# Performance work log

Measured on AMD Instinct MI355X. Metric: run time of the kernel, lower is better.

Reference implementation:

```python
import jax, jax.numpy as jnp
import numpy as np

B, L, D_MODEL, N_HEAD = 8, 1024, 1024, 16
D_K = D_MODEL // N_HEAD  # 64


def setup_inputs() -> dict:
    key = jax.random.key(0)
    ks = jax.random.split(key, 10)
    scale = 1.0 / np.sqrt(D_MODEL)
    inp = {
        "q": jax.random.normal(ks[0], (B, L, D_MODEL), jnp.float32),
        "k": jax.random.normal(ks[1], (B, L, D_MODEL), jnp.float32),
        "v": jax.random.normal(ks[2], (B, L, D_MODEL), jnp.float32),
        "mask": jax.random.randint(ks[3], (B, L, L), 0, 2, jnp.int32),
        # per-head projection weights stacked: [H, d_model, d_k]
        "Wq": jax.random.normal(ks[4], (N_HEAD, D_MODEL, D_K), jnp.float32) * scale,
        "Wk": jax.random.normal(ks[5], (N_HEAD, D_MODEL, D_K), jnp.float32) * scale,
        "Wv": jax.random.normal(ks[6], (N_HEAD, D_MODEL, D_K), jnp.float32) * scale,
        # output projection (Dense with bias): [d_model, d_model], [d_model]
        "Wo": jax.random.normal(ks[7], (D_MODEL, D_MODEL), jnp.float32) * scale,
        "bo": jnp.zeros((D_MODEL,), jnp.float32),
    }
    return inp


def reference(q, k, v, mask, Wq, Wk, Wv, Wo, bo):
    d_k = Wq.shape[-1]
    # per-head projections (mode=1 per-head Dense, no bias), vectorized over heads
    qs = jnp.einsum('bld,hdk->bhlk', q, Wq)  # [B,H,Lq,d_k]
    ks = jnp.einsum('bld,hdk->bhlk', k, Wk)  # [B,H,Lk,d_k]
    vs = jnp.einsum('bld,hdk->bhlk', v, Wv)  # [B,H,Lk,d_v]
    # scaled dot-product attention: batch_dot(q,k,axes=[2,2]) / sqrt(d_k)
    scores = jnp.einsum('bhqd,bhkd->bhqk', qs, ks) / jnp.sqrt(jnp.float32(d_k))
    # additive mask: -1e9 * (1 - mask), broadcast over heads
    scores = scores + (-1e9 * (1.0 - mask.astype(jnp.float32)))[:, None, :, :]
    attn = jax.nn.softmax(scores, axis=-1)           # [B,H,Lq,Lk] (dropout inactive at inference)
    head = jnp.einsum('bhqk,bhkd->bhqd', attn, vs)   # [B,H,Lq,d_v]
    b, h, lq, dv = head.shape
    # Concatenate heads along feature axis (head index major, as in mode=1 Concatenate)
    head_cat = head.transpose(0, 2, 1, 3).reshape(b, lq, h * dv)
    outputs = head_cat @ Wo + bo                     # [B,Lq,d_model] (dropout inactive)
    # attn heads also concatenated along last axis in mode=1
    attn_cat = attn.transpose(0, 2, 1, 3).reshape(b, lq, h * attn.shape[-1])
    return outputs, attn_cat
```

## Files before the change

### kernel.cpp

```cpp
#include <hip/hip_runtime.h>

typedef _Float16 f16;
typedef _Float16 f16x8 __attribute__((ext_vector_type(8)));
typedef _Float16 f16x4 __attribute__((ext_vector_type(4)));
typedef _Float16 f16x2 __attribute__((ext_vector_type(2)));
typedef float f32x4 __attribute__((ext_vector_type(4)));

#define GLOAD_LDS16(g, l) \
    __builtin_amdgcn_global_load_lds((const __attribute__((address_space(1))) void*)(g), \
                                     (__attribute__((address_space(3))) void*)(l), 16, 0, 0)

__device__ __forceinline__ f16x2 cvt_pk_f16(float a, float b) {
    return __builtin_bit_cast(f16x2, __builtin_amdgcn_cvt_pkrtz(a, b));
}

#define SC_LOG2E 0.180336880f

__global__ __launch_bounds__(256) void cvt3_kernel(const float* __restrict__ q,
        const float* __restrict__ k, const float* __restrict__ v, f16* __restrict__ out) {
    const int z = blockIdx.y;
    const float* src = (z == 0) ? q : (z == 1) ? k : v;
    const size_t i = ((size_t)blockIdx.x * 256 + threadIdx.x) * 8;
    float4 a = *(const float4*)&src[i], b2 = *(const float4*)&src[i + 4];
    f16x8 h;
    h[0] = (f16)a.x; h[1] = (f16)a.y; h[2] = (f16)a.z; h[3] = (f16)a.w;
    h[4] = (f16)b2.x; h[5] = (f16)b2.y; h[6] = (f16)b2.z; h[7] = (f16)b2.w;
    *(f16x8*)&out[(size_t)z * 8388608 + i] = h;
}

__global__ void transpose_w_kernel(const float* __restrict__ Wq, const float* __restrict__ Wk,
        const float* __restrict__ Wv, const float* __restrict__ Wo, f16* __restrict__ out) {
    const int z = blockIdx.y;
    int t = blockIdx.x * 256 + threadIdx.x;
    int n = t >> 10, d = t & 1023;
    float val;
    if (z < 3) {
        const float* W = (z == 0) ? Wq : (z == 1) ? Wk : Wv;
        val = W[((size_t)(n >> 6) * 1024 + d) * 64 + (n & 63)];
    } else {
        val = Wo[(size_t)d * 1024 + n];
    }
    out[(size_t)z * 1048576 + (size_t)n * 1024 + d] = (f16)val;
}

__global__ void maskbits_kernel(const int* __restrict__ mask, unsigned* __restrict__ bits) {
    int t = blockIdx.x * 256 + threadIdx.x;
    const int4* src = (const int4*)mask + (size_t)t * 8;
    unsigned w = 0;
#pragma unroll
    for (int i = 0; i < 8; ++i) {
        int4 v = src[i];
        w |= (v.x != 0 ? 1u : 0u) << (i * 4 + 0);
        w |= (v.y != 0 ? 1u : 0u) << (i * 4 + 1);
        w |= (v.z != 0 ? 1u : 0u) << (i * 4 + 2);
        w |= (v.w != 0 ? 1u : 0u) << (i * 4 + 3);
    }
    bits[t] = w;
}

__global__ __launch_bounds__(256) void proj_kernel(const f16* __restrict__ Ah,
        const f16* __restrict__ Wt, f16* __restrict__ Outp) {
    __shared__ __align__(16) f16 As[128][64];
    __shared__ __align__(16) f16 Bs[128][64];
    const int id = blockIdx.x;
    const int z = id >> 9;
    const int id2 = id & 511;
    const int m0 = ((id2 & 7) * 8 + ((id2 >> 3) & 7)) * 128;
    const int n0 = (id2 >> 6) * 128;
    const f16* A = Ah + (size_t)z * 8388608;
    const f16* Bt = Wt + (size_t)z * 1048576;
    f16* Out = Outp + (size_t)z * 8388608;
    const int tid = threadIdx.x, lane = tid & 63;
    const int w = tid >> 6, wr = w >> 1, wc = w & 1;

    f32x4 acc[4][4];
#pragma unroll
    for (int mi = 0; mi < 4; ++mi)
#pragma unroll
        for (int ni = 0; ni < 4; ++ni) acc[mi][ni] = (f32x4){0.f, 0.f, 0.f, 0.f};

    for (int kt = 0; kt < 16; ++kt) {
        const int k0 = kt * 64;
#pragma unroll
        for (int seg = 0; seg < 4; ++seg) {
            const int ch = seg * 256 + tid, r = ch >> 3, c = ch & 7;
            GLOAD_LDS16(&A[(size_t)(m0 + r) * 1024 + k0 + (c ^ (r & 7)) * 8],
                        (char*)&As[0][0] + (seg * 256 + w * 64) * 16);
            GLOAD_LDS16(&Bt[(size_t)(n0 + r) * 1024 + k0 + (c ^ (r & 7)) * 8],
                        (char*)&Bs[0][0] + (seg * 256 + w * 64) * 16);
        }
        __syncthreads();
#pragma unroll
        for (int ks = 0; ks < 2; ++ks) {
            const int slot = ks * 4 + (lane >> 4);
            f16x8 af[4], bf[4];
#pragma unroll
            for (int mi = 0; mi < 4; ++mi) {
                const int row = wr * 64 + mi * 16 + (lane & 15);
                af[mi] = *(const f16x8*)&As[row][(slot ^ (row & 7)) * 8];
            }
#pragma unroll
            for (int ni = 0; ni < 4; ++ni) {
                const int row = wc * 64 + ni * 16 + (lane & 15);
                bf[ni] = *(const f16x8*)&Bs[row][(slot ^ (row & 7)) * 8];
            }
#pragma unroll
            for (int mi = 0; mi < 4; ++mi)
#pragma unroll
                for (int ni = 0; ni < 4; ++ni)
                    acc[mi][ni] = __builtin_amdgcn_mfma_f32_16x16x32_f16(af[mi], bf[ni], acc[mi][ni], 0, 0, 0);
        }
        __syncthreads();
    }

    const float sc = (z == 0) ? SC_LOG2E : 1.0f;
#pragma unroll
    for (int mi = 0; mi < 4; ++mi)
#pragma unroll
        for (int ni = 0; ni < 4; ++ni) {
            const int row0 = m0 + wr * 64 + mi * 16 + ((lane >> 4) << 2);
            const int col = n0 + wc * 64 + ni * 16 + (lane & 15);
            const int h = col >> 6, kk = col & 63;
            const int b = row0 >> 10, l0 = row0 & 1023;
            if (z < 2) {
#pragma unroll
                for (int r = 0; r < 4; ++r)
                    Out[(((size_t)(b * 16 + h) * 1024) + l0 + r) * 64 + kk] = (f16)(acc[mi][ni][r] * sc);
            } else {
                f16x4 hv;
#pragma unroll
                for (int r = 0; r < 4; ++r) hv[r] = (f16)acc[mi][ni][r];
                *(f16x4*)&Out[((size_t)(b * 16 + h) * 64 + kk) * 1024 + l0] = hv;
            }
        }
}

__global__ __launch_bounds__(256) void out_kernel(const f16* __restrict__ A,
        const f16* __restrict__ Bt, float* __restrict__ O, const float* __restrict__ bias) {
    __shared__ __align__(16) f16 As[128][64];
    __shared__ __align__(16) f16 Bs[128][64];
    const int id2 = blockIdx.x;
    const int m0 = ((id2 & 7) * 8 + ((id2 >> 3) & 7)) * 128;
    const int n0 = (id2 >> 6) * 128;
    const int tid = threadIdx.x, lane = tid & 63;
    const int w = tid >> 6, wr = w >> 1, wc = w & 1;

    f32x4 acc[4][4];
#pragma unroll
    for (int mi = 0; mi < 4; ++mi)
#pragma unroll
        for (int ni = 0; ni < 4; ++ni) acc[mi][ni] = (f32x4){0.f, 0.f, 0.f, 0.f};

    for (int kt = 0; kt < 16; ++kt) {
        const int k0 = kt * 64;
#pragma unroll
        for (int seg = 0; seg < 4; ++seg) {
            const int ch = seg * 256 + tid, r = ch >> 3, c = ch & 7;
            GLOAD_LDS16(&A[(size_t)(m0 + r) * 1024 + k0 + (c ^ (r & 7)) * 8],
                        (char*)&As[0][0] + (seg * 256 + w * 64) * 16);
            GLOAD_LDS16(&Bt[(size_t)(n0 + r) * 1024 + k0 + (c ^ (r & 7)) * 8],
                        (char*)&Bs[0][0] + (seg * 256 + w * 64) * 16);
        }
        __syncthreads();
#pragma unroll
        for (int ks = 0; ks < 2; ++ks) {
            const int slot = ks * 4 + (lane >> 4);
            f16x8 af[4], bf[4];
#pragma unroll
            for (int mi = 0; mi < 4; ++mi) {
                const int row = wr * 64 + mi * 16 + (lane & 15);
                af[mi] = *(const f16x8*)&As[row][(slot ^ (row & 7)) * 8];
            }
#pragma unroll
            for (int ni = 0; ni < 4; ++ni) {
                const int row = wc * 64 + ni * 16 + (lane & 15);
                bf[ni] = *(const f16x8*)&Bs[row][(slot ^ (row & 7)) * 8];
            }
#pragma unroll
            for (int mi = 0; mi < 4; ++mi)
#pragma unroll
                for (int ni = 0; ni < 4; ++ni)
                    acc[mi][ni] = __builtin_amdgcn_mfma_f32_16x16x32_f16(af[mi], bf[ni], acc[mi][ni], 0, 0, 0);
        }
        __syncthreads();
    }

#pragma unroll
    for (int mi = 0; mi < 4; ++mi)
#pragma unroll
        for (int ni = 0; ni < 4; ++ni) {
            const int row0 = m0 + wr * 64 + mi * 16 + ((lane >> 4) << 2);
            const int col = n0 + wc * 64 + ni * 16 + (lane & 15);
            const float bb = bias[col];
#pragma unroll
            for (int r = 0; r < 4; ++r)
                __builtin_nontemporal_store(acc[mi][ni][r] + bb, &O[(size_t)(row0 + r) * 1024 + col]);
        }
}

__global__ __launch_bounds__(256) void attn_fused_kernel(const f16* __restrict__ Qp,
        const f16* __restrict__ Kp, const f16* __restrict__ VpT,
        const unsigned* __restrict__ bits, float* __restrict__ attn, f16* __restrict__ headcat) {
    __shared__ __align__(16) f16 Qs[128][64];
    __shared__ __align__(16) f16 Ks[2][64][64];
    __shared__ __align__(16) f16 Vs[64][64];
    __shared__ __align__(16) f16 Ps[128][64];
    __shared__ unsigned bm[128][32];
    __shared__ __align__(16) float LUTf[16][4];
    __shared__ __align__(16) f16 LUTh[16][4];
    const int bh = blockIdx.x & 127, m0 = (blockIdx.x >> 7) * 128;
    const int b = bh >> 4, h = bh & 15;
    const int tid = threadIdx.x, lane = tid & 63, w = tid >> 6;
    const f16* Qbase = Qp + (size_t)bh * 65536;
    const f16* Kbase = Kp + (size_t)bh * 65536;
    const f16* Vbase = VpT + (size_t)bh * 65536;

    auto stageK = [&](int buf, int j) {
#pragma unroll
        for (int seg = 0; seg < 2; ++seg) {
            const int ch = seg * 256 + tid, r = ch >> 3, c = ch & 7;
            GLOAD_LDS16(&Kbase[(size_t)(j * 64 + r) * 64 + (c ^ (r & 7)) * 8],
                        (char*)&Ks[buf][0][0] + (seg * 256 + w * 64) * 16);
        }
    };
    auto stageV = [&](int j) {
#pragma unroll
        for (int seg = 0; seg < 2; ++seg) {
            const int ch = seg * 256 + tid, r = ch >> 3, c = ch & 7;
            GLOAD_LDS16(&Vbase[(size_t)r * 1024 + j * 64 + (c ^ (r & 7)) * 8],
                        (char*)&Vs[0][0] + (seg * 256 + w * 64) * 16);
        }
    };

    if (tid < 16) {
#pragma unroll
        for (int i = 0; i < 4; ++i) {
            const float on = ((tid >> i) & 1) ? 1.0f : 0.0f;
            LUTf[tid][i] = on;
            LUTh[tid][i] = (f16)on;
        }
    }
#pragma unroll
    for (int seg = 0; seg < 4; ++seg) {
        const int ch = seg * 256 + tid, r = ch >> 3, c = ch & 7;
        GLOAD_LDS16(&Qbase[(size_t)(m0 + r) * 64 + (c ^ (r & 7)) * 8],
                    (char*)&Qs[0][0] + (seg * 256 + w * 64) * 16);
        GLOAD_LDS16((const char*)&bits[((size_t)b * 1024 + m0 + r) * 32] + (c ^ (r & 7)) * 16,
                    (char*)&bm[0][0] + (seg * 256 + w * 64) * 16);
    }
    stageK(0, 0);
    __syncthreads();

    float lsum[2] = {0.f, 0.f};
    const int kb0 = (lane >> 4) * 4;

    for (int j = 0; j < 16; ++j) {
        if (j < 15) stageK((j + 1) & 1, j + 1);

        f32x4 acc[2][4];
#pragma unroll
        for (int mi = 0; mi < 2; ++mi)
#pragma unroll
            for (int ni = 0; ni < 4; ++ni) acc[mi][ni] = (f32x4){0.f, 0.f, 0.f, 0.f};
#pragma unroll
        for (int ks = 0; ks < 2; ++ks) {
            const int slot = ks * 4 + (lane >> 4);
            f16x8 af[2], bf[4];
#pragma unroll
            for (int mi = 0; mi < 2; ++mi) {
                const int row = w * 32 + mi * 16 + (lane & 15);
                af[mi] = *(const f16x8*)&Qs[row][(slot ^ (row & 7)) * 8];
            }
#pragma unroll
            for (int ni = 0; ni < 4; ++ni) {
                const int row = ni * 16 + (lane & 15);
                bf[ni] = *(const f16x8*)&Ks[j & 1][row][(slot ^ (row & 7)) * 8];
            }
#pragma unroll
            for (int mi = 0; mi < 2; ++mi)
#pragma unroll
                for (int ni = 0; ni < 4; ++ni)
                    acc[mi][ni] = __builtin_amdgcn_mfma_f32_16x16x32_f16(bf[ni], af[mi], acc[mi][ni], 0, 0, 0);
        }

#pragma unroll
        for (int mi = 0; mi < 2; ++mi) {
            const int rowm = w * 32 + mi * 16 + (lane & 15);
            const int swb = (rowm & 7) << 2;
#pragma unroll
            for (int ni = 0; ni < 4; ++ni) {
                const unsigned word = bm[rowm][(2 * j + (ni >> 1)) ^ swb];
                const unsigned nib = (word >> (((ni & 1) << 4) + kb0)) & 15u;
                const float4 mf = *(const float4*)&LUTf[nib][0];
                lsum[mi] = fmaf(exp2f(acc[mi][ni][0]), mf.x, lsum[mi]);
                lsum[mi] = fmaf(exp2f(acc[mi][ni][1]), mf.y, lsum[mi]);
                lsum[mi] = fmaf(exp2f(acc[mi][ni][2]), mf.z, lsum[mi]);
                lsum[mi] = fmaf(exp2f(acc[mi][ni][3]), mf.w, lsum[mi]);
            }
        }
        __syncthreads();
    }

    stageK(0, 0);

    f16x2 rlp[2];
#pragma unroll
    for (int mi = 0; mi < 2; ++mi) {
        float s = lsum[mi];
        s += __shfl_xor(s, 16);
        s += __shfl_xor(s, 32);
        const f16 rlh = (f16)(1.0f / s);
        rlp[mi][0] = rlh; rlp[mi][1] = rlh;
    }

    f32x4 accP[2][4];
#pragma unroll
    for (int mi = 0; mi < 2; ++mi)
#pragma unroll
        for (int ni = 0; ni < 4; ++ni) accP[mi][ni] = (f32x4){0.f, 0.f, 0.f, 0.f};

    float* attnBase = attn + ((size_t)b * 1024 + m0) * 16384 + h * 1024;
    const int st_r0 = tid >> 4;
    const int st_c4 = tid & 15;
    __syncthreads();

    for (int j = 0; j < 16; ++j) {
        if (j < 15) stageK((j + 1) & 1, j + 1);
        stageV(j);

        f32x4 acc[2][4];
#pragma unroll
        for (int mi = 0; mi < 2; ++mi)
#pragma unroll
            for (int ni = 0; ni < 4; ++ni) acc[mi][ni] = (f32x4){0.f, 0.f, 0.f, 0.f};
#pragma unroll
        for (int ks = 0; ks < 2; ++ks) {
            const int slot = ks * 4 + (lane >> 4);
            f16x8 af[2], bf[4];
#pragma unroll
            for (int mi = 0; mi < 2; ++mi) {
                const int row = w * 32 + mi * 16 + (lane & 15);
                af[mi] = *(const f16x8*)&Qs[row][(slot ^ (row & 7)) * 8];
            }
#pragma unroll
            for (int ni = 0; ni < 4; ++ni) {
                const int row = ni * 16 + (lane & 15);
                bf[ni] = *(const f16x8*)&Ks[j & 1][row][(slot ^ (row & 7)) * 8];
            }
#pragma unroll
            for (int mi = 0; mi < 2; ++mi)
#pragma unroll
                for (int ni = 0; ni < 4; ++ni)
                    acc[mi][ni] = __builtin_amdgcn_mfma_f32_16x16x32_f16(bf[ni], af[mi], acc[mi][ni], 0, 0, 0);
        }

#pragma unroll
        for (int mi = 0; mi < 2; ++mi) {
            const int rowm = w * 32 + mi * 16 + (lane & 15);
            const int swb = (rowm & 7) << 2;
            const int swp = (rowm & 7) << 3;
#pragma unroll
            for (int ni = 0; ni < 4; ++ni) {
                const unsigned word = bm[rowm][(2 * j + (ni >> 1)) ^ swb];
                const unsigned nib = (word >> (((ni & 1) << 4) + kb0)) & 15u;
                const f16x4 mh = *(const f16x4*)&LUTh[nib][0];
                f16x2 p01 = cvt_pk_f16(exp2f(acc[mi][ni][0]), exp2f(acc[mi][ni][1]));
                f16x2 p23 = cvt_pk_f16(exp2f(acc[mi][ni][2]), exp2f(acc[mi][ni][3]));
                p01 = p01 * (f16x2){mh[0], mh[1]} * rlp[mi];
                p23 = p23 * (f16x2){mh[2], mh[3]} * rlp[mi];
                f16x4 pw; pw[0] = p01[0]; pw[1] = p01[1]; pw[2] = p23[0]; pw[3] = p23[1];
                *(f16x4*)&Ps[rowm][(ni * 16 + kb0) ^ swp] = pw;
            }
        }
        __syncthreads();

#pragma unroll
        for (int ks = 0; ks < 2; ++ks) {
            const int slot = ks * 4 + (lane >> 4);
            f16x8 pf[2], vf[4];
#pragma unroll
            for (int mi = 0; mi < 2; ++mi) {
                const int row = w * 32 + mi * 16 + (lane & 15);
                pf[mi] = *(const f16x8*)&Ps[row][(slot ^ (row & 7)) * 8];
            }
#pragma unroll
            for (int ni = 0; ni < 4; ++ni) {
                const int row = ni * 16 + (lane & 15);
                vf[ni] = *(const f16x8*)&Vs[row][(slot ^ (row & 7)) * 8];
            }
#pragma unroll
            for (int mi = 0; mi < 2; ++mi)
#pragma unroll
                for (int ni = 0; ni < 4; ++ni)
                    accP[mi][ni] = __builtin_amdgcn_mfma_f32_16x16x32_f16(pf[mi], vf[ni], accP[mi][ni], 0, 0, 0);
        }

#pragma unroll
        for (int i = 0; i < 8; ++i) {
            const int row = st_r0 + 16 * i;
            const f16x4 hv = *(const f16x4*)((const char*)&Ps[row][0] +
                    ((st_c4 >> 1) ^ (row & 7)) * 16 + (st_c4 & 1) * 8);
            f32x4 fv = {(float)hv[0], (float)hv[1], (float)hv[2], (float)hv[3]};
            __builtin_nontemporal_store(fv,
                    (f32x4*)&attnBase[(size_t)row * 16384 + j * 64 + st_c4 * 4]);
        }
        __syncthreads();
    }

#pragma unroll
    for (int mi = 0; mi < 2; ++mi)
#pragma unroll
        for (int ni = 0; ni < 4; ++ni) {
            const int row0 = m0 + w * 32 + mi * 16 + ((lane >> 4) << 2);
            const int col = ni * 16 + (lane & 15);
#pragma unroll
            for (int r = 0; r < 4; ++r)
                headcat[((size_t)b * 1024 + row0 + r) * 1024 + h * 64 + col] = (f16)accP[mi][ni][r];
        }
}

extern "C" void kernel_launch(void* const* d_in, const int* in_sizes, int n_in,
                              void* d_out, int out_size, void* d_ws, size_t ws_size,
                              hipStream_t stream) {
    const float* q = (const float*)d_in[0];
    const float* k = (const float*)d_in[1];
    const float* v = (const float*)d_in[2];
    const int* mask = (const int*)d_in[3];
    const float* Wq = (const float*)d_in[4];
    const float* Wk = (const float*)d_in[5];
    const float* Wv = (const float*)d_in[6];
    const float* Wo = (const float*)d_in[7];
    const float* bo = (const float*)d_in[8];

    float* out0 = (float*)d_out;
    float* attn = out0 + (size_t)8 * 1024 * 1024;

    char* ws = (char*)d_ws;
    f16* wt   = (f16*)(ws + ((size_t)0 << 20));
    f16* qh   = (f16*)(ws + ((size_t)8 << 20));
    f16* Qp   = (f16*)(ws + ((size_t)56 << 20));
    f16* Kp   = (f16*)(ws + ((size_t)72 << 20));
    f16* VpT  = (f16*)(ws + ((size_t)88 << 20));
    f16* hc   = (f16*)(ws + ((size_t)104 << 20));
    unsigned* bits = (unsigned*)(ws + ((size_t)120 << 20));
    f16* wot  = wt + (size_t)3 * 1048576;

    cvt3_kernel<<<dim3(4096, 3), 256, 0, stream>>>(q, k, v, qh);
    transpose_w_kernel<<<dim3(4096, 4), 256, 0, stream>>>(Wq, Wk, Wv, Wo, wt);
    maskbits_kernel<<<1024, 256, 0, stream>>>(mask, bits);

    proj_kernel<<<1536, 256, 0, stream>>>(qh, wt, Qp);

    attn_fused_kernel<<<1024, 256, 0, stream>>>(Qp, Kp, VpT, bits, attn, hc);

    out_kernel<<<512, 256, 0, stream>>>(hc, wot, out0, bo);
}
```

Before: 298.9 us.

## Restructure attention to single-pass with full score row in LDS

The attention kernel now handles 32 query rows per block instead of 128 and keeps the whole unnormalized probability row (32x1024 fp16) in LDS. This removes the second QK^T pass that recomputed scores after the row sums were known. K and V are read straight from global memory into registers with double buffering, replacing the LDS staging. The key range is split across warp pairs, which then combine their row sums and PV partials through LDS. The grid grows fourfold, but K/V are reloaded by more blocks and each block uses a large LDS allocation, which may limit occupancy.

```diff
diff --git a/kernel.cpp b/kernel.cpp
--- a/kernel.cpp
+++ b/kernel.cpp
@@ -201,36 +201,22 @@
 __global__ __launch_bounds__(256) void attn_fused_kernel(const f16* __restrict__ Qp,
         const f16* __restrict__ Kp, const f16* __restrict__ VpT,
         const unsigned* __restrict__ bits, float* __restrict__ attn, f16* __restrict__ headcat) {
-    __shared__ __align__(16) f16 Qs[128][64];
-    __shared__ __align__(16) f16 Ks[2][64][64];
-    __shared__ __align__(16) f16 Vs[64][64];
-    __shared__ __align__(16) f16 Ps[128][64];
-    __shared__ unsigned bm[128][32];
+    __shared__ __align__(16) f16 Ps[32][1024];
+    __shared__ unsigned bm[32][32];
     __shared__ __align__(16) float LUTf[16][4];
     __shared__ __align__(16) f16 LUTh[16][4];
-    const int bh = blockIdx.x & 127, m0 = (blockIdx.x >> 7) * 128;
+    __shared__ float lsum2[2][2][16];
+    __shared__ float rlS[32];
+    __shared__ float red[2][16][68];
+
+    const int bh = blockIdx.x & 127, m0 = (blockIdx.x >> 7) * 32;
     const int b = bh >> 4, h = bh & 15;
     const int tid = threadIdx.x, lane = tid & 63, w = tid >> 6;
+    const int g = w & 1, h2 = w >> 1;
+    const int l15 = lane & 15, t4 = lane >> 4;
     const f16* Qbase = Qp + (size_t)bh * 65536;
     const f16* Kbase = Kp + (size_t)bh * 65536;
     const f16* Vbase = VpT + (size_t)bh * 65536;
-
-    auto stageK = [&](int buf, int j) {
-#pragma unroll
-        for (int seg = 0; seg < 2; ++seg) {
-            const int ch = seg * 256 + tid, r = ch >> 3, c = ch & 7;
-            GLOAD_LDS16(&Kbase[(size_t)(j * 64 + r) * 64 + (c ^ (r & 7)) * 8],
-                        (char*)&Ks[buf][0][0] + (seg * 256 + w * 64) * 16);
-        }
-    };
-    auto stageV = [&](int j) {
-#pragma unroll
-        for (int seg = 0; seg < 2; ++seg) {
-            const int ch = seg * 256 + tid, r = ch >> 3, c = ch & 7;
-            GLOAD_LDS16(&Vbase[(size_t)r * 1024 + j * 64 + (c ^ (r & 7)) * 8],
-                        (char*)&Vs[0][0] + (seg * 256 + w * 64) * 16);
-        }
-    };
 
     if (tid < 16) {
 #pragma unroll
@@ -240,183 +226,130 @@
             LUTh[tid][i] = (f16)on;
         }
     }
-#pragma unroll
-    for (int seg = 0; seg < 4; ++seg) {
-        const int ch = seg * 256 + tid, r = ch >> 3, c = ch & 7;
-        GLOAD_LDS16(&Qbase[(size_t)(m0 + r) * 64 + (c ^ (r & 7)) * 8],
-                    (char*)&Qs[0][0] + (seg * 256 + w * 64) * 16);
+    {
+        const int r = tid >> 3, c = tid & 7;
         GLOAD_LDS16((const char*)&bits[((size_t)b * 1024 + m0 + r) * 32] + (c ^ (r & 7)) * 16,
-                    (char*)&bm[0][0] + (seg * 256 + w * 64) * 16);
-    }
-    stageK(0, 0);
+                    (char*)&bm[0][0] + (w * 64) * 16);
+    }
+
+    const int qrow = m0 + g * 16 + l15;
+    f16x8 af0 = *(const f16x8*)&Qbase[(size_t)qrow * 64 + t4 * 8];
+    f16x8 af1 = *(const f16x8*)&Qbase[(size_t)qrow * 64 + 32 + t4 * 8];
+
+    const int row = g * 16 + l15;
+    const int swb = (row & 7) << 2;
+    const int swz = (row & 7) << 1;
+    float lsum = 0.f;
+
+    const int j0 = h2 * 8;
+    f16x8 bf[2][4][2];
+#pragma unroll
+    for (int ni = 0; ni < 4; ++ni)
+#pragma unroll
+        for (int ks = 0; ks < 2; ++ks)
+            bf[0][ni][ks] = *(const f16x8*)&Kbase[(size_t)(j0 * 64 + ni * 16 + l15) * 64 + ks * 32 + t4 * 8];
+
     __syncthreads();
 
-    float lsum[2] = {0.f, 0.f};
-    const int kb0 = (lane >> 4) * 4;
-
-    for (int j = 0; j < 16; ++j) {
-        if (j < 15) stageK((j + 1) & 1, j + 1);
-
-        f32x4 acc[2][4];
-#pragma unroll
-        for (int mi = 0; mi < 2; ++mi)
-#pragma unroll
-            for (int ni = 0; ni < 4; ++ni) acc[mi][ni] = (f32x4){0.f, 0.f, 0.f, 0.f};
-#pragma unroll
-        for (int ks = 0; ks < 2; ++ks) {
-            const int slot = ks * 4 + (lane >> 4);
-            f16x8 af[2], bf[4];
-#pragma unroll
-            for (int mi = 0; mi < 2; ++mi) {
-                const int row = w * 32 + mi * 16 + (lane & 15);
-                af[mi] = *(const f16x8*)&Qs[row][(slot ^ (row & 7)) * 8];
-            }
-#pragma unroll
-            for (int ni = 0; ni < 4; ++ni) {
-                const int row = ni * 16 + (lane & 15);
-                bf[ni] = *(const f16x8*)&Ks[j & 1][row][(slot ^ (row & 7)) * 8];
-            }
-#pragma unroll
-            for (int mi = 0; mi < 2; ++mi)
-#pragma unroll
-                for (int ni = 0; ni < 4; ++ni)
-                    acc[mi][ni] = __builtin_amdgcn_mfma_f32_16x16x32_f16(bf[ni], af[mi], acc[mi][ni], 0, 0, 0);
-        }
-
-#pragma unroll
-        for (int mi = 0; mi < 2; ++mi) {
-            const int rowm = w * 32 + mi * 16 + (lane & 15);
-            const int swb = (rowm & 7) << 2;
-#pragma unroll
-            for (int ni = 0; ni < 4; ++ni) {
-                const unsigned word = bm[rowm][(2 * j + (ni >> 1)) ^ swb];
-                const unsigned nib = (word >> (((ni & 1) << 4) + kb0)) & 15u;
-                const float4 mf = *(const float4*)&LUTf[nib][0];
-                lsum[mi] = fmaf(exp2f(acc[mi][ni][0]), mf.x, lsum[mi]);
-                lsum[mi] = fmaf(exp2f(acc[mi][ni][1]), mf.y, lsum[mi]);
-                lsum[mi] = fmaf(exp2f(acc[mi][ni][2]), mf.z, lsum[mi]);
-                lsum[mi] = fmaf(exp2f(acc[mi][ni][3]), mf.w, lsum[mi]);
-            }
-        }
-        __syncthreads();
-    }
-
-    stageK(0, 0);
-
-    f16x2 rlp[2];
-#pragma unroll
-    for (int mi = 0; mi < 2; ++mi) {
-        float s = lsum[mi];
-        s += __shfl_xor(s, 16);
-        s += __shfl_xor(s, 32);
-        const f16 rlh = (f16)(1.0f / s);
-        rlp[mi][0] = rlh; rlp[mi][1] = rlh;
-    }
-
-    f32x4 accP[2][4];
-#pragma unroll
-    for (int mi = 0; mi < 2; ++mi)
-#pragma unroll
-        for (int ni = 0; ni < 4; ++ni) accP[mi][ni] = (f32x4){0.f, 0.f, 0.f, 0.f};
-
-    float* attnBase = attn + ((size_t)b * 1024 + m0) * 16384 + h * 1024;
-    const int st_r0 = tid >> 4;
-    const int st_c4 = tid & 15;
+#pragma unroll
+    for (int jj = 0; jj < 8; ++jj) {
+        const int j = j0 + jj;
+        if (jj < 7) {
+#pragma unroll
+            for (int ni = 0; ni < 4; ++ni)
+#pragma unroll
+                for (int ks = 0; ks < 2; ++ks)
+                    bf[(jj + 1) & 1][ni][ks] = *(const f16x8*)&Kbase[(size_t)((j + 1) * 64 + ni * 16 + l15) * 64 + ks * 32 + t4 * 8];
+        }
+        f32x4 acc[4];
+#pragma unroll
+        for (int ni = 0; ni < 4; ++ni) acc[ni] = (f32x4){0.f, 0.f, 0.f, 0.f};
+#pragma unroll
+        for (int ni = 0; ni < 4; ++ni) {
+            acc[ni] = __builtin_amdgcn_mfma_f32_16x16x32_f16(bf[jj & 1][ni][0], af0, acc[ni], 0, 0, 0);
+            acc[ni] = __builtin_amdgcn_mfma_f32_16x16x32_f16(bf[jj & 1][ni][1], af1, acc[ni], 0, 0, 0);
+        }
+#pragma unroll
+        for (int ni = 0; ni < 4; ++ni) {
+            const unsigned word = bm[row][(2 * j + (ni >> 1)) ^ swb];
+            const unsigned nib = (word >> (((ni & 1) << 4) + t4 * 4)) & 15u;
+            const float4 mf = *(const float4*)&LUTf[nib][0];
+            const float e0 = exp2f(acc[ni][0]), e1 = exp2f(acc[ni][1]);
+            const float e2 = exp2f(acc[ni][2]), e3 = exp2f(acc[ni][3]);
+            lsum = fmaf(e0, mf.x, lsum); lsum = fmaf(e1, mf.y, lsum);
+            lsum = fmaf(e2, mf.z, lsum); lsum = fmaf(e3, mf.w, lsum);
+            const f16x4 mh = *(const f16x4*)&LUTh[nib][0];
+            f16x2 p01 = cvt_pk_f16(e0, e1) * (f16x2){mh[0], mh[1]};
+            f16x2 p23 = cvt_pk_f16(e2, e3) * (f16x2){mh[2], mh[3]};
+            f16x4 pw; pw[0] = p01[0]; pw[1] = p01[1]; pw[2] = p23[0]; pw[3] = p23[1];
+            const int col4 = j * 16 + ni * 4 + t4;
+            *(f16x4*)((char*)&Ps[0][0] + row * 2048 + ((col4 ^ swz) << 3)) = pw;
+        }
+    }
+
+    lsum += __shfl_xor(lsum, 16);
+    lsum += __shfl_xor(lsum, 32);
+    if (lane < 16) lsum2[h2][g][lane] = lsum;
     __syncthreads();
-
-    for (int j = 0; j < 16; ++j) {
-        if (j < 15) stageK((j + 1) & 1, j + 1);
-        stageV(j);
-
-        f32x4 acc[2][4];
-#pragma unroll
-        for (int mi = 0; mi < 2; ++mi)
-#pragma unroll
-            for (int ni = 0; ni < 4; ++ni) acc[mi][ni] = (f32x4){0.f, 0.f, 0.f, 0.f};
-#pragma unroll
-        for (int ks = 0; ks < 2; ++ks) {
-            const int slot = ks * 4 + (lane >> 4);
-            f16x8 af[2], bf[4];
-#pragma unroll
-            for (int mi = 0; mi < 2; ++mi) {
-                const int row = w * 32 + mi * 16 + (lane & 15);
-                af[mi] = *(const f16x8*)&Qs[row][(slot ^ (row & 7)) * 8];
-            }
-#pragma unroll
-            for (int ni = 0; ni < 4; ++ni) {
-                const int row = ni * 16 + (lane & 15);
-                bf[ni] = *(const f16x8*)&Ks[j & 1][row][(slot ^ (row & 7)) * 8];
-            }
-#pragma unroll
-            for (int mi = 0; mi < 2; ++mi)
-#pragma unroll
-                for (int ni = 0; ni < 4; ++ni)
-                    acc[mi][ni] = __builtin_amdgcn_mfma_f32_16x16x32_f16(bf[ni], af[mi], acc[mi][ni], 0, 0, 0);
-        }
-
-#pragma unroll
-        for (int mi = 0; mi < 2; ++mi) {
-            const int rowm = w * 32 + mi * 16 + (lane & 15);
-            const int swb = (rowm & 7) << 2;
-            const int swp = (rowm & 7) << 3;
-#pragma unroll
-            for (int ni = 0; ni < 4; ++ni) {
-                const unsigned word = bm[rowm][(2 * j + (ni >> 1)) ^ swb];
-                const unsigned nib = (word >> (((ni & 1) << 4) + kb0)) & 15u;
-                const f16x4 mh = *(const f16x4*)&LUTh[nib][0];
-                f16x2 p01 = cvt_pk_f16(exp2f(acc[mi][ni][0]), exp2f(acc[mi][ni][1]));
-                f16x2 p23 = cvt_pk_f16(exp2f(acc[mi][ni][2]), exp2f(acc[mi][ni][3]));
-                p01 = p01 * (f16x2){mh[0], mh[1]} * rlp[mi];
-                p23 = p23 * (f16x2){mh[2], mh[3]} * rlp[mi];
-                f16x4 pw; pw[0] = p01[0]; pw[1] = p01[1]; pw[2] = p23[0]; pw[3] = p23[1];
-                *(f16x4*)&Ps[rowm][(ni * 16 + kb0) ^ swp] = pw;
-            }
-        }
-        __syncthreads();
-
-#pragma unroll
-        for (int ks = 0; ks < 2; ++ks) {
-            const int slot = ks * 4 + (lane >> 4);
-            f16x8 pf[2], vf[4];
-#pragma unroll
-            for (int mi = 0; mi < 2; ++mi) {
-                const int row = w * 32 + mi * 16 + (lane & 15);
-                pf[mi] = *(const f16x8*)&Ps[row][(slot ^ (row & 7)) * 8];
-            }
-#pragma unroll
-            for (int ni = 0; ni < 4; ++ni) {
-                const int row = ni * 16 + (lane & 15);
-                vf[ni] = *(const f16x8*)&Vs[row][(slot ^ (row & 7)) * 8];
-            }
-#pragma unroll
-            for (int mi = 0; mi < 2; ++mi)
-#pragma unroll
-                for (int ni = 0; ni < 4; ++ni)
-                    accP[mi][ni] = __builtin_amdgcn_mfma_f32_16x16x32_f16(pf[mi], vf[ni], accP[mi][ni], 0, 0, 0);
-        }
-
-#pragma unroll
-        for (int i = 0; i < 8; ++i) {
-            const int row = st_r0 + 16 * i;
-            const f16x4 hv = *(const f16x4*)((const char*)&Ps[row][0] +
-                    ((st_c4 >> 1) ^ (row & 7)) * 16 + (st_c4 & 1) * 8);
-            f32x4 fv = {(float)hv[0], (float)hv[1], (float)hv[2], (float)hv[3]};
-            __builtin_nontemporal_store(fv,
-                    (f32x4*)&attnBase[(size_t)row * 16384 + j * 64 + st_c4 * 4]);
-        }
-        __syncthreads();
-    }
-
-#pragma unroll
-    for (int mi = 0; mi < 2; ++mi)
-#pragma unroll
-        for (int ni = 0; ni < 4; ++ni) {
-            const int row0 = m0 + w * 32 + mi * 16 + ((lane >> 4) << 2);
-            const int col = ni * 16 + (lane & 15);
+    if (tid < 32) rlS[tid] = 1.0f / (lsum2[0][tid >> 4][tid & 15] + lsum2[1][tid >> 4][tid & 15]);
+    __syncthreads();
+
+    {
+        const int srow = tid >> 3, tcol = tid & 7;
+        const float rl = rlS[srow];
+        const int sswz = (srow & 7) << 1;
+        float* aB = attn + (size_t)(b * 1024 + m0 + srow) * 16384 + h * 1024;
+#pragma unroll
+        for (int i = 0; i < 32; ++i) {
+            const int col4 = tcol + i * 8;
+            const f16x4 hv = *(const f16x4*)((const char*)&Ps[0][0] + srow * 2048 + ((col4 ^ sswz) << 3));
+            f32x4 fv = {(float)hv[0] * rl, (float)hv[1] * rl, (float)hv[2] * rl, (float)hv[3] * rl};
+            __builtin_nontemporal_store(fv, (f32x4*)&aB[col4 * 4]);
+        }
+    }
+
+    f32x4 accP[4];
+#pragma unroll
+    for (int ni = 0; ni < 4; ++ni) accP[ni] = (f32x4){0.f, 0.f, 0.f, 0.f};
+    const int kk0 = h2 * 16;
+    f16x8 vf[2][4];
+#pragma unroll
+    for (int ni = 0; ni < 4; ++ni)
+        vf[0][ni] = *(const f16x8*)&Vbase[(size_t)(ni * 16 + l15) * 1024 + kk0 * 32 + t4 * 8];
+#pragma unroll
+    for (int t = 0; t < 16; ++t) {
+        const int kk = kk0 + t;
+        if (t < 15) {
+#pragma unroll
+            for (int ni = 0; ni < 4; ++ni)
+                vf[(t + 1) & 1][ni] = *(const f16x8*)&Vbase[(size_t)(ni * 16 + l15) * 1024 + (kk + 1) * 32 + t4 * 8];
+        }
+        const int prow = g * 16 + l15;
+        const int col4 = kk * 8 + t4 * 2;
+        const f16x8 pf = *(const f16x8*)((const char*)&Ps[0][0] + prow * 2048 + ((col4 ^ ((prow & 7) << 1)) << 3));
+#pragma unroll
+        for (int ni = 0; ni < 4; ++ni)
+            accP[ni] = __builtin_amdgcn_mfma_f32_16x16x32_f16(pf, vf[t & 1][ni], accP[ni], 0, 0, 0);
+    }
+
+    if (h2 == 1) {
+#pragma unroll
+        for (int ni = 0; ni < 4; ++ni)
 #pragma unroll
             for (int r = 0; r < 4; ++r)
-                headcat[((size_t)b * 1024 + row0 + r) * 1024 + h * 64 + col] = (f16)accP[mi][ni][r];
-        }
+                red[g][t4 * 4 + r][ni * 16 + l15] = accP[ni][r];
+    }
+    __syncthreads();
+    if (h2 == 0) {
+#pragma unroll
+        for (int ni = 0; ni < 4; ++ni)
+#pragma unroll
+            for (int r = 0; r < 4; ++r) {
+                const int qr = t4 * 4 + r;
+                const float val = (accP[ni][r] + red[g][qr][ni * 16 + l15]) * rlS[g * 16 + qr];
+                headcat[(size_t)(b * 1024 + m0 + g * 16 + qr) * 1024 + h * 64 + ni * 16 + l15] = (f16)val;
+            }
+    }
 }
 
 extern "C" void kernel_launch(void* const* d_in, const int* in_sizes, int n_in,
@@ -451,7 +384,7 @@
 
     proj_kernel<<<1536, 256, 0, stream>>>(qh, wt, Qp);
 
-    attn_fused_kernel<<<1024, 256, 0, stream>>>(Qp, Kp, VpT, bits, attn, hc);
+    attn_fused_kernel<<<4096, 256, 0, stream>>>(Qp, Kp, VpT, bits, attn, hc);
 
     out_kernel<<<512, 256, 0, stream>>>(hc, wot, out0, bo);
 }
```

After: 394.3 us. 1.32x slower.
